# Kernel optimization log

Measured on AMD Instinct MI355X. Metric: run time of the kernel, lower is better.

The kernel has to match this reference:

```python
import jax, jax.numpy as jnp
import numpy as np

EPS = 1e-5

def gamma_layer_norm(x, gamma):
    # LayerNorm over last dim with learnable gamma only (no bias)
    mu = jnp.mean(x, axis=-1, keepdims=True)
    var = jnp.var(x, axis=-1, keepdims=True)
    return (x - mu) * jax.lax.rsqrt(var + EPS) * gamma

def setup_inputs() -> dict:
    key = jax.random.key(0)
    k1, k2, k3, k4 = jax.random.split(key, 4)
    b, n, dim = 8, 4096, 512
    heads, head_size = 8, 64
    hidden = heads * head_size  # 512
    x = jax.random.normal(k1, (b, n, dim), dtype=jnp.float32)
    # nn.Linear(dim, hidden*3, bias=False): weight [3*hidden, dim]
    w_qkv = jax.random.normal(k2, (3 * hidden, dim), dtype=jnp.float32) * (dim ** -0.5)
    # nn.Linear(hidden, dim, bias=False): weight [dim, hidden]
    w_out = jax.random.normal(k3, (dim, hidden), dtype=jnp.float32) * (hidden ** -0.5)
    gamma = 1.0 + 0.02 * jax.random.normal(k4, (dim,), dtype=jnp.float32)
    return {"x": x, "w_qkv": w_qkv, "w_out": w_out, "gamma": gamma}

def reference(x, w_qkv, w_out, gamma):
    b, n, dim = x.shape
    heads, head_size = 8, 64
    scale = head_size ** -0.5
    # norm=False -> Identity; no time conditioning
    qkv = jnp.einsum('bnd,hd->bnh', x, w_qkv)  # [b, n, 3*hidden]
    q, k, v = jnp.split(qkv, 3, axis=-1)
    def to_heads(t):
        return t.reshape(b, n, heads, head_size).transpose(0, 2, 1, 3)  # b h n d
    q, k, v = to_heads(q), to_heads(k), to_heads(v)
    q = jax.nn.softmax(q, axis=-1) * scale   # softmax over feature dim
    k = jax.nn.softmax(k, axis=-2)           # softmax over sequence dim
    context = jnp.einsum('bhnd,bhne->bhde', k, v)      # [b, h, d, e]
    out = jnp.einsum('bhde,bhnd->bhne', context, q)    # [b, h, n, e]
    out = out.transpose(0, 2, 1, 3).reshape(b, n, heads * head_size)
    out = jnp.einsum('bnh,dh->bnd', out, w_out)
    out = gamma_layer_norm(out, gamma)  # dropout inactive (p=0 / eval)
    return out
```

## Files before the change

### kernel.cpp

```cpp
#include <hip/hip_runtime.h>
#include <hip/hip_bf16.h>
#include <stdint.h>
#include <stddef.h>

typedef __bf16 bf16_t;
typedef __bf16 bf16x8 __attribute__((ext_vector_type(8)));
typedef __bf16 bf16x4 __attribute__((ext_vector_type(4)));
typedef float floatx4 __attribute__((ext_vector_type(4)));

#define DIM 512
#define SEQ 4096
#define BATCH 8
#define LDP 40

static __device__ __forceinline__ floatx4 mfma_bf16(bf16x8 a, bf16x8 b, floatx4 c) {
  return __builtin_amdgcn_mfma_f32_16x16x32_bf16(a, b, c, 0, 0, 0);
}

__global__ __launch_bounds__(256) void k_cvt_w(const float* __restrict__ w, bf16_t* __restrict__ wb) {
  int i = (blockIdx.x * 256 + threadIdx.x) * 8;
  float4 a = *(const float4*)&w[i];
  float4 b = *(const float4*)&w[i + 4];
  bf16x8 o;
  o[0] = (bf16_t)a.x; o[1] = (bf16_t)a.y; o[2] = (bf16_t)a.z; o[3] = (bf16_t)a.w;
  o[4] = (bf16_t)b.x; o[5] = (bf16_t)b.y; o[6] = (bf16_t)b.z; o[7] = (bf16_t)b.w;
  *(bf16x8*)&wb[i] = o;
}

__global__ __launch_bounds__(256) void k_qkv(const float* __restrict__ X,
                                             const bf16_t* __restrict__ Wb,
                                             bf16_t* __restrict__ qs,
                                             bf16_t* __restrict__ ek,
                                             bf16_t* __restrict__ vb,
                                             float* __restrict__ S) {
  __shared__ __align__(16) bf16_t As[128 * LDP];
  __shared__ __align__(16) bf16_t Bs[128 * LDP];
  const int tid = threadIdx.x;
  const int lane = tid & 63;
  const int wid = tid >> 6;
  const int wr = wid >> 1, wc = wid & 1;
  const int l15 = lane & 15, l4 = lane >> 4;
  const int m0 = blockIdx.x * 128;
  const int n0 = blockIdx.y * 128;

  floatx4 acc[4][4];
#pragma unroll
  for (int i = 0; i < 4; ++i)
#pragma unroll
    for (int j = 0; j < 4; ++j) acc[i][j] = (floatx4){0.f, 0.f, 0.f, 0.f};

  for (int kt = 0; kt < DIM; kt += 32) {
#pragma unroll
    for (int i = 0; i < 4; ++i) {
      int q = tid + i * 256;
      int row = q >> 3;
      int c4 = (q & 7) << 2;
      float4 f = *(const float4*)&X[(size_t)(m0 + row) * DIM + kt + c4];
      bf16x4 h;
      h[0] = (bf16_t)f.x; h[1] = (bf16_t)f.y; h[2] = (bf16_t)f.z; h[3] = (bf16_t)f.w;
      *(bf16x4*)&As[row * LDP + c4] = h;
    }
#pragma unroll
    for (int i = 0; i < 2; ++i) {
      int q = tid + i * 256;
      int row = q >> 2;
      int c8 = (q & 3) << 3;
      *(bf16x8*)&Bs[row * LDP + c8] = *(const bf16x8*)&Wb[(size_t)(n0 + row) * DIM + kt + c8];
    }
    __syncthreads();
    bf16x8 af[4], bfr[4];
#pragma unroll
    for (int f = 0; f < 4; ++f) {
      af[f]  = *(const bf16x8*)&As[(wr * 64 + f * 16 + l15) * LDP + l4 * 8];
      bfr[f] = *(const bf16x8*)&Bs[(wc * 64 + f * 16 + l15) * LDP + l4 * 8];
    }
#pragma unroll
    for (int i = 0; i < 4; ++i)
#pragma unroll
      for (int j = 0; j < 4; ++j)
        acc[i][j] = mfma_bf16(af[i], bfr[j], acc[i][j]);
    __syncthreads();
  }

  const int colbase = n0 + wc * 64;
  if (n0 < 512) {
#pragma unroll
    for (int fm = 0; fm < 4; ++fm) {
#pragma unroll
      for (int r = 0; r < 4; ++r) {
        float v0 = acc[fm][0][r], v1 = acc[fm][1][r], v2 = acc[fm][2][r], v3 = acc[fm][3][r];
        float mx = fmaxf(fmaxf(v0, v1), fmaxf(v2, v3));
        mx = fmaxf(mx, __shfl_xor(mx, 1));
        mx = fmaxf(mx, __shfl_xor(mx, 2));
        mx = fmaxf(mx, __shfl_xor(mx, 4));
        mx = fmaxf(mx, __shfl_xor(mx, 8));
        float e0 = __expf(v0 - mx), e1 = __expf(v1 - mx), e2 = __expf(v2 - mx), e3 = __expf(v3 - mx);
        float s = e0 + e1 + e2 + e3;
        s += __shfl_xor(s, 1); s += __shfl_xor(s, 2); s += __shfl_xor(s, 4); s += __shfl_xor(s, 8);
        float inv = 0.125f / s;
        int m = m0 + wr * 64 + fm * 16 + l4 * 4 + r;
        bf16_t* rowp = qs + (size_t)m * DIM + colbase;
        rowp[l15]      = (bf16_t)(e0 * inv);
        rowp[16 + l15] = (bf16_t)(e1 * inv);
        rowp[32 + l15] = (bf16_t)(e2 * inv);
        rowp[48 + l15] = (bf16_t)(e3 * inv);
      }
    }
  } else if (n0 < 1024) {
    const int cb = colbase - 512;
    float c0 = 0.f, c1 = 0.f, c2 = 0.f, c3 = 0.f;
#pragma unroll
    for (int fm = 0; fm < 4; ++fm) {
#pragma unroll
      for (int r = 0; r < 4; ++r) {
        int m = m0 + wr * 64 + fm * 16 + l4 * 4 + r;
        bf16_t* rowp = ek + (size_t)m * DIM + cb;
        float e0 = __expf(acc[fm][0][r]);
        float e1 = __expf(acc[fm][1][r]);
        float e2 = __expf(acc[fm][2][r]);
        float e3 = __expf(acc[fm][3][r]);
        rowp[l15]      = (bf16_t)e0;
        rowp[16 + l15] = (bf16_t)e1;
        rowp[32 + l15] = (bf16_t)e2;
        rowp[48 + l15] = (bf16_t)e3;
        c0 += e0; c1 += e1; c2 += e2; c3 += e3;
      }
    }
    c0 += __shfl_xor(c0, 16); c0 += __shfl_xor(c0, 32);
    c1 += __shfl_xor(c1, 16); c1 += __shfl_xor(c1, 32);
    c2 += __shfl_xor(c2, 16); c2 += __shfl_xor(c2, 32);
    c3 += __shfl_xor(c3, 16); c3 += __shfl_xor(c3, 32);
    if (lane < 16) {
      int b = m0 >> 12;
      atomicAdd(&S[b * 512 + cb + lane],      c0);
      atomicAdd(&S[b * 512 + cb + 16 + lane], c1);
      atomicAdd(&S[b * 512 + cb + 32 + lane], c2);
      atomicAdd(&S[b * 512 + cb + 48 + lane], c3);
    }
  } else {
    const int cb = colbase - 1024;
#pragma unroll
    for (int fm = 0; fm < 4; ++fm) {
#pragma unroll
      for (int r = 0; r < 4; ++r) {
        int m = m0 + wr * 64 + fm * 16 + l4 * 4 + r;
        bf16_t* rowp = vb + (size_t)m * DIM + cb;
        rowp[l15]      = (bf16_t)acc[fm][0][r];
        rowp[16 + l15] = (bf16_t)acc[fm][1][r];
        rowp[32 + l15] = (bf16_t)acc[fm][2][r];
        rowp[48 + l15] = (bf16_t)acc[fm][3][r];
      }
    }
  }
}

#define TP 136
__global__ __launch_bounds__(256) void k_ctx(const bf16_t* __restrict__ ek,
                                             const bf16_t* __restrict__ vb,
                                             float* __restrict__ ctxpart) {
  __shared__ __align__(16) bf16_t ekT[64 * TP];
  __shared__ __align__(16) bf16_t vT[64 * TP];
  __shared__ float red[4096];
  const int tid = threadIdx.x;
  const int lane = tid & 63, wid = tid >> 6;
  const int l15 = lane & 15, l4 = lane >> 4;
  const int bh = blockIdx.x, chunk = blockIdx.y;
  const int b = bh >> 3, h = bh & 7;
  const int base = b * SEQ + chunk * 512;

  floatx4 acc[4][4];
#pragma unroll
  for (int i = 0; i < 4; ++i)
#pragma unroll
    for (int j = 0; j < 4; ++j) acc[i][j] = (floatx4){0.f, 0.f, 0.f, 0.f};

  for (int nt = 0; nt < 4; ++nt) {
    const int n0 = base + nt * 128;
#pragma unroll
    for (int i = 0; i < 4; ++i) {
      int q = tid + i * 256;
      int n = q & 127;
      int c8 = (q >> 7) << 3;
      bf16x8 vk = *(const bf16x8*)&ek[(size_t)(n0 + n) * DIM + h * 64 + c8];
      bf16x8 vv = *(const bf16x8*)&vb[(size_t)(n0 + n) * DIM + h * 64 + c8];
#pragma unroll
      for (int j = 0; j < 8; ++j) {
        ekT[(c8 + j) * TP + n] = vk[j];
        vT [(c8 + j) * TP + n] = vv[j];
      }
    }
    __syncthreads();
    const int nb = wid * 32;
    bf16x8 af[4], bfr[4];
#pragma unroll
    for (int f = 0; f < 4; ++f) {
      af[f]  = *(const bf16x8*)&ekT[(f * 16 + l15) * TP + nb + l4 * 8];
      bfr[f] = *(const bf16x8*)&vT [(f * 16 + l15) * TP + nb + l4 * 8];
    }
#pragma unroll
    for (int i = 0; i < 4; ++i)
#pragma unroll
      for (int j = 0; j < 4; ++j)
        acc[i][j] = mfma_bf16(af[i], bfr[j], acc[i][j]);
    __syncthreads();
  }

  for (int w = 0; w < 4; ++w) {
    if (wid == w) {
#pragma unroll
      for (int fm = 0; fm < 4; ++fm)
#pragma unroll
        for (int fn = 0; fn < 4; ++fn)
#pragma unroll
          for (int r = 0; r < 4; ++r) {
            int d = fm * 16 + l4 * 4 + r;
            int e = fn * 16 + l15;
            if (w == 0) red[d * 64 + e] = acc[fm][fn][r];
            else        red[d * 64 + e] += acc[fm][fn][r];
          }
    }
    __syncthreads();
  }
  float* dst = ctxpart + ((size_t)bh * 8 + chunk) * 4096;
#pragma unroll
  for (int i = 0; i < 4; ++i) {
    int q = tid + i * 256;
    *(float4*)&dst[q * 4] = *(const float4*)&red[q * 4];
  }
}

__global__ __launch_bounds__(256) void k_ctxred(const float* __restrict__ ctxpart,
                                                const float* __restrict__ S,
                                                float* __restrict__ ctx) {
  int bh = blockIdx.x;
  int idx = blockIdx.y * 256 + threadIdx.x;
  int b = bh >> 3, h = bh & 7;
  float s = 0.f;
#pragma unroll
  for (int p = 0; p < 8; ++p) s += ctxpart[((size_t)bh * 8 + p) * 4096 + idx];
  int d = idx >> 6;
  ctx[(size_t)bh * 4096 + idx] = s / S[b * 512 + h * 64 + d];
}

__global__ __launch_bounds__(128) void k_mt(const float* __restrict__ ctx,
                                            const float* __restrict__ w_out,
                                            bf16_t* __restrict__ Mt) {
  __shared__ float cs[4096];
  const int tid = threadIdx.x;
  const int b = blockIdx.x, h = blockIdx.y, dq = blockIdx.z;
#pragma unroll
  for (int i = 0; i < 8; ++i) {
    int q = tid + i * 128;
    *(float4*)&cs[q * 4] = *(const float4*)&ctx[((size_t)(b * 8 + h)) * 4096 + q * 4];
  }
  __syncthreads();
  const int dcol = dq * 128 + tid;
  float a[64];
#pragma unroll
  for (int d = 0; d < 64; ++d) a[d] = 0.f;
  for (int e = 0; e < 64; ++e) {
    float we = w_out[(size_t)dcol * 512 + h * 64 + e];
#pragma unroll
    for (int d = 0; d < 64; ++d) a[d] += cs[d * 64 + e] * we;
  }
  bf16_t* dst = Mt + ((size_t)b * 512 + dcol) * 512 + h * 64;
#pragma unroll
  for (int g = 0; g < 8; ++g) {
    bf16x8 o;
#pragma unroll
    for (int j = 0; j < 8; ++j) o[j] = (bf16_t)a[g * 8 + j];
    *(bf16x8*)&dst[g * 8] = o;
  }
}

__global__ __launch_bounds__(256) void k_out(const bf16_t* __restrict__ qs,
                                             const bf16_t* __restrict__ Mt,
                                             float* __restrict__ out2) {
  __shared__ __align__(16) bf16_t As[128 * LDP];
  __shared__ __align__(16) bf16_t Bs[128 * LDP];
  const int tid = threadIdx.x;
  const int lane = tid & 63, wid = tid >> 6;
  const int wr = wid >> 1, wc = wid & 1;
  const int l15 = lane & 15, l4 = lane >> 4;
  const int m0 = blockIdx.x * 128;
  const int n0 = blockIdx.y * 128;
  const bf16_t* Bp = Mt + (size_t)(blockIdx.x >> 5) * 512 * 512;

  floatx4 acc[4][4];
#pragma unroll
  for (int i = 0; i < 4; ++i)
#pragma unroll
    for (int j = 0; j < 4; ++j) acc[i][j] = (floatx4){0.f, 0.f, 0.f, 0.f};

  for (int kt = 0; kt < 512; kt += 32) {
#pragma unroll
    for (int i = 0; i < 2; ++i) {
      int q = tid + i * 256;
      int row = q >> 2;
      int c8 = (q & 3) << 3;
      *(bf16x8*)&As[row * LDP + c8] = *(const bf16x8*)&qs[(size_t)(m0 + row) * 512 + kt + c8];
      *(bf16x8*)&Bs[row * LDP + c8] = *(const bf16x8*)&Bp[(size_t)(n0 + row) * 512 + kt + c8];
    }
    __syncthreads();
    bf16x8 af[4], bfr[4];
#pragma unroll
    for (int f = 0; f < 4; ++f) {
      af[f]  = *(const bf16x8*)&As[(wr * 64 + f * 16 + l15) * LDP + l4 * 8];
      bfr[f] = *(const bf16x8*)&Bs[(wc * 64 + f * 16 + l15) * LDP + l4 * 8];
    }
#pragma unroll
    for (int i = 0; i < 4; ++i)
#pragma unroll
      for (int j = 0; j < 4; ++j)
        acc[i][j] = mfma_bf16(af[i], bfr[j], acc[i][j]);
    __syncthreads();
  }
#pragma unroll
  for (int fm = 0; fm < 4; ++fm) {
#pragma unroll
    for (int r = 0; r < 4; ++r) {
      int m = m0 + wr * 64 + fm * 16 + l4 * 4 + r;
      float* rowp = out2 + (size_t)m * 512 + n0 + wc * 64;
      rowp[l15]      = acc[fm][0][r];
      rowp[16 + l15] = acc[fm][1][r];
      rowp[32 + l15] = acc[fm][2][r];
      rowp[48 + l15] = acc[fm][3][r];
    }
  }
}

__global__ __launch_bounds__(256) void k_ln(const float* __restrict__ out2,
                                            const float* __restrict__ gamma,
                                            float* __restrict__ out) {
  const int lane = threadIdx.x & 63;
  const int row = blockIdx.x * 4 + (threadIdx.x >> 6);
  const float* x = out2 + (size_t)row * 512;
  float4 v0 = ((const float4*)x)[lane];
  float4 v1 = ((const float4*)x)[lane + 64];
  float s = v0.x + v0.y + v0.z + v0.w + v1.x + v1.y + v1.z + v1.w;
  float q = v0.x * v0.x + v0.y * v0.y + v0.z * v0.z + v0.w * v0.w
          + v1.x * v1.x + v1.y * v1.y + v1.z * v1.z + v1.w * v1.w;
#pragma unroll
  for (int m = 1; m <= 32; m <<= 1) { s += __shfl_xor(s, m); q += __shfl_xor(q, m); }
  float mean = s * (1.f / 512.f);
  float var = q * (1.f / 512.f) - mean * mean;
  float rstd = rsqrtf(var + 1e-5f);
  float4 g0 = ((const float4*)gamma)[lane];
  float4 g1 = ((const float4*)gamma)[lane + 64];
  float4 o0, o1;
  o0.x = (v0.x - mean) * rstd * g0.x;
  o0.y = (v0.y - mean) * rstd * g0.y;
  o0.z = (v0.z - mean) * rstd * g0.z;
  o0.w = (v0.w - mean) * rstd * g0.w;
  o1.x = (v1.x - mean) * rstd * g1.x;
  o1.y = (v1.y - mean) * rstd * g1.y;
  o1.z = (v1.z - mean) * rstd * g1.z;
  o1.w = (v1.w - mean) * rstd * g1.w;
  float* y = out + (size_t)row * 512;
  ((float4*)y)[lane] = o0;
  ((float4*)y)[lane + 64] = o1;
}

extern "C" void kernel_launch(void* const* d_in, const int* in_sizes, int n_in,
                              void* d_out, int out_size, void* d_ws, size_t ws_size,
                              hipStream_t stream) {
  const float* x     = (const float*)d_in[0];
  const float* w_qkv = (const float*)d_in[1];
  const float* w_out = (const float*)d_in[2];
  const float* gamma = (const float*)d_in[3];
  float* out = (float*)d_out;
  char* ws = (char*)d_ws;

  bf16_t* qs      = (bf16_t*)(ws);
  bf16_t* ek      = (bf16_t*)(ws + 33554432);
  bf16_t* vb      = (bf16_t*)(ws + 67108864);
  bf16_t* wqkvb   = (bf16_t*)(ws + 100663296);
  float*  S       = (float*)(ws + 102236160);
  float*  ctx     = (float*)(ws + 102252544);
  float*  ctxpart = (float*)(ws + 103301120);
  bf16_t* Mt      = (bf16_t*)(ws + 111689728);
  float*  out2    = (float*)(ws + 33554432);

  hipMemsetAsync(S, 0, BATCH * 512 * sizeof(float), stream);

  k_cvt_w<<<384, 256, 0, stream>>>(w_qkv, wqkvb);

  dim3 g1(256, 12);
  k_qkv<<<g1, 256, 0, stream>>>(x, wqkvb, qs, ek, vb, S);

  dim3 g2(64, 8);
  k_ctx<<<g2, 256, 0, stream>>>(ek, vb, ctxpart);

  dim3 g3(64, 16);
  k_ctxred<<<g3, 256, 0, stream>>>(ctxpart, S, ctx);

  dim3 g4(8, 8, 4);
  k_mt<<<g4, 128, 0, stream>>>(ctx, w_out, Mt);

  dim3 g5(256, 4);
  k_out<<<g5, 256, 0, stream>>>(qs, Mt, out2);

  k_ln<<<8192, 256, 0, stream>>>(out2, gamma, out);
}
```

Measured before the change: 212.8 us.

## Use direct global-to-LDS loads with XOR-swizzled tiles in QKV and output GEMMs

Replaces the register-staged global loads and LDS stores in the QKV and output-projection GEMMs with global_load_lds 16-byte direct transfers into unpadded, XOR-swizzled shared tiles. In the QKV kernel, X now lands in LDS as fp32 and is converted to bf16 after the fragment read, which doubles the A-tile LDS footprint and adds conversion work in the inner loop. The goal is to cut VGPR traffic and instruction count for staging. The swizzle aims to avoid the bank conflicts that padding used to prevent. There is still no double buffering, so each k-step keeps its two barriers.

```diff
diff --git a/kernel.cpp b/kernel.cpp
--- a/kernel.cpp
+++ b/kernel.cpp
@@ -11,10 +11,17 @@
 #define DIM 512
 #define SEQ 4096
 #define BATCH 8
+#define BK 32
 #define LDP 40
 
 static __device__ __forceinline__ floatx4 mfma_bf16(bf16x8 a, bf16x8 b, floatx4 c) {
   return __builtin_amdgcn_mfma_f32_16x16x32_bf16(a, b, c, 0, 0, 0);
+}
+
+typedef __attribute__((address_space(1))) const void* gas_ptr;
+typedef __attribute__((address_space(3))) void* las_ptr;
+static __device__ __forceinline__ void gll16(const void* g, void* l) {
+  __builtin_amdgcn_global_load_lds((gas_ptr)g, (las_ptr)l, 16, 0, 0);
 }
 
 __global__ __launch_bounds__(256) void k_cvt_w(const float* __restrict__ w, bf16_t* __restrict__ wb) {
@@ -33,46 +40,53 @@
                                              bf16_t* __restrict__ ek,
                                              bf16_t* __restrict__ vb,
                                              float* __restrict__ S) {
-  __shared__ __align__(16) bf16_t As[128 * LDP];
-  __shared__ __align__(16) bf16_t Bs[128 * LDP];
+  __shared__ __align__(16) float  Asf[128 * BK];
+  __shared__ __align__(16) bf16_t Bs [128 * BK];
   const int tid = threadIdx.x;
   const int lane = tid & 63;
-  const int wid = tid >> 6;
-  const int wr = wid >> 1, wc = wid & 1;
+  const int w = tid >> 6;
+  const int wr = w >> 1, wc = w & 1;
   const int l15 = lane & 15, l4 = lane >> 4;
   const int m0 = blockIdx.x * 128;
   const int n0 = blockIdx.y * 128;
 
+  const float* gA = X + (size_t)(m0 + w * 32 + (lane >> 3)) * DIM
+                      + (((lane & 7) ^ (lane >> 3)) << 2);
+  const bf16_t* gB = Wb + (size_t)(n0 + w * 32 + (lane >> 2)) * DIM
+                        + ((((lane & 3) ^ ((lane >> 2) & 3))) << 3);
+  float*  lA = &Asf[(w * 32) * BK];
+  bf16_t* lB = &Bs [(w * 32) * BK];
+
   floatx4 acc[4][4];
 #pragma unroll
   for (int i = 0; i < 4; ++i)
 #pragma unroll
     for (int j = 0; j < 4; ++j) acc[i][j] = (floatx4){0.f, 0.f, 0.f, 0.f};
 
-  for (int kt = 0; kt < DIM; kt += 32) {
-#pragma unroll
-    for (int i = 0; i < 4; ++i) {
-      int q = tid + i * 256;
-      int row = q >> 3;
-      int c4 = (q & 7) << 2;
-      float4 f = *(const float4*)&X[(size_t)(m0 + row) * DIM + kt + c4];
-      bf16x4 h;
-      h[0] = (bf16_t)f.x; h[1] = (bf16_t)f.y; h[2] = (bf16_t)f.z; h[3] = (bf16_t)f.w;
-      *(bf16x4*)&As[row * LDP + c4] = h;
-    }
-#pragma unroll
-    for (int i = 0; i < 2; ++i) {
-      int q = tid + i * 256;
-      int row = q >> 2;
-      int c8 = (q & 3) << 3;
-      *(bf16x8*)&Bs[row * LDP + c8] = *(const bf16x8*)&Wb[(size_t)(n0 + row) * DIM + kt + c8];
-    }
+  for (int kt = 0; kt < DIM; kt += BK) {
+    gll16(gA,            lA);
+    gll16(gA + 8 * DIM,  lA + 8 * BK);
+    gll16(gA + 16 * DIM, lA + 16 * BK);
+    gll16(gA + 24 * DIM, lA + 24 * BK);
+    gll16(gB,            lB);
+    gll16(gB + 16 * DIM, lB + 16 * BK);
+    gA += BK; gB += BK;
     __syncthreads();
     bf16x8 af[4], bfr[4];
 #pragma unroll
     for (int f = 0; f < 4; ++f) {
-      af[f]  = *(const bf16x8*)&As[(wr * 64 + f * 16 + l15) * LDP + l4 * 8];
-      bfr[f] = *(const bf16x8*)&Bs[(wc * 64 + f * 16 + l15) * LDP + l4 * 8];
+      int ar = wr * 64 + f * 16 + l15;
+      int u0 = (l4 * 2) ^ (ar & 7);
+      int u1 = (l4 * 2 + 1) ^ (ar & 7);
+      float4 a0 = *(const float4*)&Asf[ar * BK + u0 * 4];
+      float4 a1 = *(const float4*)&Asf[ar * BK + u1 * 4];
+      bf16x8 t;
+      t[0] = (bf16_t)a0.x; t[1] = (bf16_t)a0.y; t[2] = (bf16_t)a0.z; t[3] = (bf16_t)a0.w;
+      t[4] = (bf16_t)a1.x; t[5] = (bf16_t)a1.y; t[6] = (bf16_t)a1.z; t[7] = (bf16_t)a1.w;
+      af[f] = t;
+      int br = wc * 64 + f * 16 + l15;
+      int bu = l4 ^ (br & 3);
+      bfr[f] = *(const bf16x8*)&Bs[br * BK + bu * 8];
     }
 #pragma unroll
     for (int i = 0; i < 4; ++i)
@@ -276,37 +290,45 @@
 __global__ __launch_bounds__(256) void k_out(const bf16_t* __restrict__ qs,
                                              const bf16_t* __restrict__ Mt,
                                              float* __restrict__ out2) {
-  __shared__ __align__(16) bf16_t As[128 * LDP];
-  __shared__ __align__(16) bf16_t Bs[128 * LDP];
+  __shared__ __align__(16) bf16_t As2[128 * BK];
+  __shared__ __align__(16) bf16_t Bs2[128 * BK];
   const int tid = threadIdx.x;
-  const int lane = tid & 63, wid = tid >> 6;
-  const int wr = wid >> 1, wc = wid & 1;
+  const int lane = tid & 63, w = tid >> 6;
+  const int wr = w >> 1, wc = w & 1;
   const int l15 = lane & 15, l4 = lane >> 4;
   const int m0 = blockIdx.x * 128;
   const int n0 = blockIdx.y * 128;
   const bf16_t* Bp = Mt + (size_t)(blockIdx.x >> 5) * 512 * 512;
 
+  const int srow = lane >> 2;
+  const int sunit = (lane & 3) ^ (srow & 3);
+  const bf16_t* gA = qs + (size_t)(m0 + w * 32 + srow) * 512 + (sunit << 3);
+  const bf16_t* gB = Bp + (size_t)(n0 + w * 32 + srow) * 512 + (sunit << 3);
+  bf16_t* lA = &As2[(w * 32) * BK];
+  bf16_t* lB = &Bs2[(w * 32) * BK];
+
   floatx4 acc[4][4];
 #pragma unroll
   for (int i = 0; i < 4; ++i)
 #pragma unroll
     for (int j = 0; j < 4; ++j) acc[i][j] = (floatx4){0.f, 0.f, 0.f, 0.f};
 
-  for (int kt = 0; kt < 512; kt += 32) {
-#pragma unroll
-    for (int i = 0; i < 2; ++i) {
-      int q = tid + i * 256;
-      int row = q >> 2;
-      int c8 = (q & 3) << 3;
-      *(bf16x8*)&As[row * LDP + c8] = *(const bf16x8*)&qs[(size_t)(m0 + row) * 512 + kt + c8];
-      *(bf16x8*)&Bs[row * LDP + c8] = *(const bf16x8*)&Bp[(size_t)(n0 + row) * 512 + kt + c8];
-    }
+  for (int kt = 0; kt < 512; kt += BK) {
+    gll16(gA,            lA);
+    gll16(gA + 16 * 512, lA + 16 * BK);
+    gll16(gB,            lB);
+    gll16(gB + 16 * 512, lB + 16 * BK);
+    gA += BK; gB += BK;
     __syncthreads();
     bf16x8 af[4], bfr[4];
 #pragma unroll
     for (int f = 0; f < 4; ++f) {
-      af[f]  = *(const bf16x8*)&As[(wr * 64 + f * 16 + l15) * LDP + l4 * 8];
-      bfr[f] = *(const bf16x8*)&Bs[(wc * 64 + f * 16 + l15) * LDP + l4 * 8];
+      int ar = wr * 64 + f * 16 + l15;
+      int au = l4 ^ (ar & 3);
+      af[f] = *(const bf16x8*)&As2[ar * BK + au * 8];
+      int br = wc * 64 + f * 16 + l15;
+      int bu = l4 ^ (br & 3);
+      bfr[f] = *(const bf16x8*)&Bs2[br * BK + bu * 8];
     }
 #pragma unroll
     for (int i = 0; i < 4; ++i)
```

Result: faster. 203.6 us (-4.3%).
